# Kernel optimization log

Hardware: AMD Instinct MI355X
Metric: run time of the kernel (lower is better)

Reference implementation:

```python
import jax, jax.numpy as jnp
import numpy as np

N_NODES = 50000
N_EDGES = 400000
IN_DIM, HID, OUT_DIM = 24, 256, 12


def _sage_conv(x, src, dst, w_l, b_l, w_r, num_nodes):
    # PyG SAGEConv (aggr='mean', root_weight=True):
    #   out = lin_l(mean_{j in N(i)} x_j) + lin_r(x_i)
    msg = x[src]                                             # [E, H] gather
    s = jax.ops.segment_sum(msg, dst, num_segments=num_nodes)  # [N, H]
    cnt = jax.ops.segment_sum(jnp.ones((src.shape[0],), x.dtype), dst,
                              num_segments=num_nodes)          # [N]
    mean = s / jnp.maximum(cnt, 1.0)[:, None]
    return mean @ w_l + b_l + x @ w_r


def setup_inputs() -> dict:
    key = jax.random.key(0)
    ks = jax.random.split(key, 16)
    sc = 0.05
    inp = {
        "x": jax.random.normal(ks[0], (N_NODES, IN_DIM), jnp.float32),
        "edge_index": jax.random.randint(ks[1], (2, N_EDGES), 0, N_NODES, jnp.int64),
        # encoder: Linear(24,128) ReLU Linear(128,256) ReLU
        "enc_w1": sc * jax.random.normal(ks[2], (IN_DIM, HID // 2), jnp.float32),
        "enc_b1": jnp.zeros((HID // 2,), jnp.float32),
        "enc_w2": sc * jax.random.normal(ks[3], (HID // 2, HID), jnp.float32),
        "enc_b2": jnp.zeros((HID,), jnp.float32),
        # SAGEConv 1 / 2: lin_l (with bias) on aggregated, lin_r (no bias) on root
        "s1_wl": sc * jax.random.normal(ks[4], (HID, HID), jnp.float32),
        "s1_bl": jnp.zeros((HID,), jnp.float32),
        "s1_wr": sc * jax.random.normal(ks[5], (HID, HID), jnp.float32),
        "s2_wl": sc * jax.random.normal(ks[6], (HID, HID), jnp.float32),
        "s2_bl": jnp.zeros((HID,), jnp.float32),
        "s2_wr": sc * jax.random.normal(ks[7], (HID, HID), jnp.float32),
        # readout: Linear(256,128) ReLU Linear(128,12)
        "ro_w1": sc * jax.random.normal(ks[8], (HID, HID // 2), jnp.float32),
        "ro_b1": jnp.zeros((HID // 2,), jnp.float32),
        "ro_w2": sc * jax.random.normal(ks[9], (HID // 2, OUT_DIM), jnp.float32),
        "ro_b2": jnp.zeros((OUT_DIM,), jnp.float32),
    }
    return inp


def reference(x, edge_index, enc_w1, enc_b1, enc_w2, enc_b2,
              s1_wl, s1_bl, s1_wr, s2_wl, s2_bl, s2_wr,
              ro_w1, ro_b1, ro_w2, ro_b2):
    n = x.shape[0]
    src, dst = edge_index[0], edge_index[1]
    # encoder MLP
    h = jax.nn.relu(x @ enc_w1 + enc_b1)
    h = jax.nn.relu(h @ enc_w2 + enc_b2)
    # two SAGE layers with ReLU
    h = jax.nn.relu(_sage_conv(h, src, dst, s1_wl, s1_bl, s1_wr, n))
    h = jax.nn.relu(_sage_conv(h, src, dst, s2_wl, s2_bl, s2_wr, n))
    # readout MLP
    h = jax.nn.relu(h @ ro_w1 + ro_b1)
    return h @ ro_w2 + ro_b2
```

## Files before the change

kernel.cpp:

```cpp
#include <hip/hip_runtime.h>
#include <hip/hip_bf16.h>

#define N_NODES 50000
#define N_EDGES 400000
#define IN_DIM 24
#define HID 256
#define OUT_DIM 12

typedef _Float16 fp16_t;
typedef __attribute__((ext_vector_type(8))) _Float16 half8;
typedef __attribute__((ext_vector_type(4))) float f32x4;

__device__ __forceinline__ void gload_lds16(const void* g, void* l) {
    typedef __attribute__((address_space(3))) unsigned int u32_lds;
    typedef const __attribute__((address_space(1))) unsigned int u32_glb;
    __builtin_amdgcn_global_load_lds((u32_glb*)(unsigned long long)g,
                                     (u32_lds*)(unsigned int)(unsigned long long)l,
                                     16, 0, 0);
}

template<int K, int M, int ROWS>
__global__ __launch_bounds__(M) void lin_enc1(const float* __restrict__ X,
                                              const float* __restrict__ W,
                                              const float* __restrict__ b,
                                              fp16_t* __restrict__ Y, int N) {
    __shared__ float xs[ROWS][K];
    const int row0 = blockIdx.x * ROWS;
    const int tid = threadIdx.x;
    for (int i = tid; i < ROWS * K; i += M) {
        int r = i / K, k = i - r * K;
        int gr = row0 + r;
        xs[r][k] = (gr < N) ? X[(long long)gr * K + k] : 0.f;
    }
    __syncthreads();
    const int j = tid;
    float acc[ROWS];
    float bj = b[j];
#pragma unroll
    for (int r = 0; r < ROWS; ++r) acc[r] = bj;
    for (int k = 0; k < K; ++k) {
        float w = W[k * M + j];
#pragma unroll
        for (int r = 0; r < ROWS; ++r) acc[r] = fmaf(xs[r][k], w, acc[r]);
    }
#pragma unroll
    for (int r = 0; r < ROWS; ++r) {
        int gr = row0 + r;
        if (gr < N) {
            float v = fmaxf(acc[r], 0.f);
            Y[(size_t)gr * M + j] = (fp16_t)v;
        }
    }
}

__global__ __launch_bounds__(256) void wtrans_all(
    const float* __restrict__ enc_w2,
    const float* __restrict__ s1_wl, const float* __restrict__ s1_wr,
    const float* __restrict__ s2_wl, const float* __restrict__ s2_wr,
    const float* __restrict__ ro_w1,
    fp16_t* __restrict__ wtE,
    fp16_t* __restrict__ wtS1,
    fp16_t* __restrict__ wtS2,
    fp16_t* __restrict__ wtR) {
    const int sE = 256 * 128, sS = 256 * 512, sR = 128 * 256;
    int idx = blockIdx.x * blockDim.x + threadIdx.x;
    float v; fp16_t* p; int o;
    if (idx < sE) {
        int j = idx / 128, k = idx - j * 128;
        v = enc_w2[(size_t)k * 256 + j]; p = wtE; o = idx;
    } else if (idx < sE + sS) {
        int t = idx - sE; int j = t / 512, k = t - j * 512;
        v = (k < 256) ? s1_wl[(size_t)k * 256 + j] : s1_wr[(size_t)(k - 256) * 256 + j];
        p = wtS1; o = t;
    } else if (idx < sE + 2 * sS) {
        int t = idx - sE - sS; int j = t / 512, k = t - j * 512;
        v = (k < 256) ? s2_wl[(size_t)k * 256 + j] : s2_wr[(size_t)(k - 256) * 256 + j];
        p = wtS2; o = t;
    } else if (idx < sE + 2 * sS + sR) {
        int t = idx - sE - 2 * sS; int j = t / 256, k = t - j * 256;
        v = ro_w1[(size_t)k * 128 + j]; p = wtR; o = t;
    } else return;
    p[o] = (fp16_t)v;
}

template<int K, int MODE, int BM, int BN, bool WF32, bool WH16, bool RELU>
__global__ __launch_bounds__((BM / 64) * (BN / 64) * 64, 4) void gemm_mfma(
    const fp16_t* __restrict__ A, const fp16_t* __restrict__ A2,
    const fp16_t* __restrict__ W,
    const float* __restrict__ bias,
    float* __restrict__ Yf, fp16_t* __restrict__ Yh,
    int N, int M) {
    constexpr int NWR = BM / 64;
    constexpr int NWC = BN / 64;
    constexpr int NT = NWR * NWC * 64;
    __shared__ __align__(16) fp16_t ldsA[BM * 32];
    __shared__ __align__(16) fp16_t ldsB[BN * 32];
    const int tid = threadIdx.x;
    const int r0 = blockIdx.x * BM;
    const int j0 = blockIdx.y * BN;
    const int w = tid >> 6, lane = tid & 63;
    const int wr = w / NWC, wc = w % NWC;
    const int lrow = lane & 15, lg = lane >> 4;

    f32x4 acc[4][4] = {};

    for (int kc = 0; kc < K; kc += 32) {
        __syncthreads();
        const fp16_t* pa;
        int ka, KA;
        if (MODE == 1) {
            KA = HID;
            if (kc >= HID) { pa = A2; ka = kc - HID; }
            else           { pa = A;  ka = kc; }
        } else {
            KA = K; pa = A; ka = kc;
        }
#pragma unroll
        for (int c = tid; c < BM * 4; c += NT) {
            int row = c >> 2, p = c & 3;
            int g = (p - (row >> 1)) & 3;
            int gr = r0 + row; if (gr > N - 1) gr = N - 1;
            gload_lds16(pa + (size_t)gr * KA + ka + g * 8,
                        (char*)ldsA + (size_t)c * 16);
        }
#pragma unroll
        for (int c = tid; c < BN * 4; c += NT) {
            int row = c >> 2, p = c & 3;
            int g = (p - (row >> 1)) & 3;
            gload_lds16(W + (size_t)(j0 + row) * K + kc + g * 8,
                        (char*)ldsB + (size_t)c * 16);
        }
        __syncthreads();

        half8 a[4], b[4];
#pragma unroll
        for (int f = 0; f < 4; ++f) {
            int ar = wr * 64 + f * 16 + lrow;
            int sa = (lg + (ar >> 1)) & 3;
            a[f] = *(const half8*)&ldsA[ar * 32 + sa * 8];
            int br = wc * 64 + f * 16 + lrow;
            int sb = (lg + (br >> 1)) & 3;
            b[f] = *(const half8*)&ldsB[br * 32 + sb * 8];
        }
#pragma unroll
        for (int fi = 0; fi < 4; ++fi)
#pragma unroll
            for (int fj = 0; fj < 4; ++fj)
                acc[fi][fj] = __builtin_amdgcn_mfma_f32_16x16x32_f16(a[fi], b[fj], acc[fi][fj], 0, 0, 0);
    }

#pragma unroll
    for (int fj = 0; fj < 4; ++fj) {
        int ocol = j0 + wc * 64 + fj * 16 + lrow;
        float bv = bias[ocol];
#pragma unroll
        for (int fi = 0; fi < 4; ++fi) {
#pragma unroll
            for (int r = 0; r < 4; ++r) {
                int orow = r0 + wr * 64 + fi * 16 + lg * 4 + r;
                if (orow < N) {
                    float v = acc[fi][fj][r] + bv;
                    if (RELU) v = fmaxf(v, 0.f);
                    size_t o = (size_t)orow * M + ocol;
                    if (WF32) Yf[o] = v;
                    if (WH16) Yh[o] = (fp16_t)v;
                }
            }
        }
    }
}

__global__ __launch_bounds__(1024) void zero_kernel(int* __restrict__ p, int n) {
    int i = blockIdx.x * blockDim.x + threadIdx.x;
    if (i < n) p[i] = 0;
}

__global__ void deg_kernel(const int* __restrict__ dst, int* __restrict__ deg, int E) {
    int e = blockIdx.x * blockDim.x + threadIdx.x;
    if (e < E) atomicAdd(&deg[dst[e]], 1);
}

__global__ __launch_bounds__(256) void scan_local(const int* __restrict__ deg,
                                                  int* __restrict__ locincl,
                                                  int* __restrict__ bsum, int N) {
    const int t = threadIdx.x;
    const int i = blockIdx.x * 256 + t;
    int v = (i < N) ? deg[i] : 0;
    const int lane = t & 63;
    int x = v;
#pragma unroll
    for (int off = 1; off < 64; off <<= 1) {
        int y = __shfl_up(x, off, 64);
        if (lane >= off) x += y;
    }
    __shared__ int wsum[4];
    if (lane == 63) wsum[t >> 6] = x;
    __syncthreads();
    const int wid = t >> 6;
    int add = 0;
    for (int wI = 0; wI < wid; ++wI) add += wsum[wI];
    x += add;
    if (i < N) locincl[i] = x;
    if (t == 255) bsum[blockIdx.x] = x;
}

__global__ __launch_bounds__(256) void scan_bsum(int* __restrict__ bsum, int B) {
    const int t = threadIdx.x;
    int v = (t < B) ? bsum[t] : 0;
    const int lane = t & 63;
    int x = v;
#pragma unroll
    for (int off = 1; off < 64; off <<= 1) {
        int y = __shfl_up(x, off, 64);
        if (lane >= off) x += y;
    }
    __shared__ int wsum[4];
    if (lane == 63) wsum[t >> 6] = x;
    __syncthreads();
    const int wid = t >> 6;
    int add = 0;
    for (int wI = 0; wI < wid; ++wI) add += wsum[wI];
    x += add;
    if (t < B) bsum[t] = x - v;
}

__global__ __launch_bounds__(256) void scan_final(const int* __restrict__ deg,
                                                  const int* __restrict__ locincl,
                                                  const int* __restrict__ bsum,
                                                  int* __restrict__ rowptr,
                                                  int* __restrict__ cursor, int N, int E) {
    const int i = blockIdx.x * 256 + threadIdx.x;
    if (i < N) {
        int excl = bsum[blockIdx.x] + locincl[i] - deg[i];
        rowptr[i] = excl;
        cursor[i] = excl;
    }
    if (i == 0) rowptr[N] = E;
}

__global__ void scatter_kernel(const int* __restrict__ src, const int* __restrict__ dst,
                               int* __restrict__ cursor, int* __restrict__ esrc, int E) {
    int e = blockIdx.x * blockDim.x + threadIdx.x;
    if (e < E) {
        int pos = atomicAdd(&cursor[dst[e]], 1);
        esrc[pos] = src[e];
    }
}

__global__ __launch_bounds__(256) void agg_csr(const fp16_t* __restrict__ h,
                                               const int* __restrict__ rowptr,
                                               const int* __restrict__ esrc,
                                               fp16_t* __restrict__ mean, int N) {
    const int n = blockIdx.x * 4 + (threadIdx.x >> 6);
    if (n >= N) return;
    const int lane = threadIdx.x & 63;
    const int half = lane >> 5;
    const int l32 = lane & 31;
    const int r0 = rowptr[n];
    const int r1 = rowptr[n + 1];
    const int deg = r1 - r0;

    float acc[8];
#pragma unroll
    for (int j = 0; j < 8; ++j) acc[j] = 0.f;

    for (int e = r0 + half; e < r1; e += 2) {
        int s = esrc[e];
        half8 v = *(const half8*)&h[(size_t)s * HID + l32 * 8];
#pragma unroll
        for (int j = 0; j < 8; ++j) acc[j] += (float)v[j];
    }
#pragma unroll
    for (int j = 0; j < 8; ++j) acc[j] += __shfl(acc[j], lane ^ 32, 64);

    if (half == 0) {
        float inv = 1.0f / fmaxf((float)deg, 1.0f);
        half8 o;
#pragma unroll
        for (int j = 0; j < 8; ++j) o[j] = (fp16_t)(acc[j] * inv);
        *(half8*)&mean[(size_t)n * HID + l32 * 8] = o;
    }
}

__global__ void lin_final(const float* __restrict__ X, const float* __restrict__ W,
                          const float* __restrict__ b, float* __restrict__ Y, int N) {
    int idx = blockIdx.x * blockDim.x + threadIdx.x;
    if (idx >= N * OUT_DIM) return;
    int row = idx / OUT_DIM;
    int j = idx - row * OUT_DIM;
    float acc = b[j];
#pragma unroll 8
    for (int k = 0; k < 128; ++k)
        acc = fmaf(X[row * 128 + k], W[k * OUT_DIM + j], acc);
    Y[idx] = acc;
}

extern "C" void kernel_launch(void* const* d_in, const int* in_sizes, int n_in,
                              void* d_out, int out_size, void* d_ws, size_t ws_size,
                              hipStream_t stream) {
    const float* x      = (const float*)d_in[0];
    const int*   eidx   = (const int*)d_in[1];
    const float* enc_w1 = (const float*)d_in[2];
    const float* enc_b1 = (const float*)d_in[3];
    const float* enc_w2 = (const float*)d_in[4];
    const float* enc_b2 = (const float*)d_in[5];
    const float* s1_wl  = (const float*)d_in[6];
    const float* s1_bl  = (const float*)d_in[7];
    const float* s1_wr  = (const float*)d_in[8];
    const float* s2_wl  = (const float*)d_in[9];
    const float* s2_bl  = (const float*)d_in[10];
    const float* s2_wr  = (const float*)d_in[11];
    const float* ro_w1  = (const float*)d_in[12];
    const float* ro_b1  = (const float*)d_in[13];
    const float* ro_w2  = (const float*)d_in[14];
    const float* ro_b2  = (const float*)d_in[15];
    float* out = (float*)d_out;

    const int N = N_NODES;
    const int E = N_EDGES;
    const int* src = eidx;
    const int* dst = eidx + E;

    char* ws = (char*)d_ws;
    size_t off = 0;
    auto alloc = [&](size_t bytes) { void* p = ws + off; off += (bytes + 255) & ~255ULL; return p; };
    int* deg     = (int*)alloc((size_t)N * 4);
    int* rowptr  = (int*)alloc((size_t)(N + 1) * 4);
    int* cursor  = (int*)alloc((size_t)N * 4);
    int* esrc    = (int*)alloc((size_t)E * 4);
    int* locincl = (int*)alloc((size_t)N * 4);
    int* bsum    = (int*)alloc((size_t)256 * 4);
    fp16_t* wtE  = (fp16_t*)alloc((size_t)256 * 128 * 2);
    fp16_t* wtS1 = (fp16_t*)alloc((size_t)256 * 512 * 2);
    fp16_t* wtS2 = (fp16_t*)alloc((size_t)256 * 512 * 2);
    fp16_t* wtR  = (fp16_t*)alloc((size_t)128 * 256 * 2);
    fp16_t* h0   = (fp16_t*)alloc((size_t)N * 128 * 2);
    float* f32buf = (float*)alloc((size_t)N * 128 * 4);
    fp16_t* hA   = (fp16_t*)alloc((size_t)N * HID * 2);
    fp16_t* hB   = (fp16_t*)alloc((size_t)N * HID * 2);
    fp16_t* mbuf = (fp16_t*)alloc((size_t)N * HID * 2);

    const int nb8 = (N + 7) / 8;
    const int gx128 = (N + 127) / 128;
    const int nbScan = (N + 255) / 256;
    const int nbAgg = (N + 3) / 4;
    const int wtTot = 256 * 128 + 2 * 256 * 512 + 128 * 256;

    zero_kernel<<<(N + 1023) / 1024, 1024, 0, stream>>>(deg, N);
    deg_kernel<<<(E + 255) / 256, 256, 0, stream>>>(dst, deg, E);
    scan_local<<<nbScan, 256, 0, stream>>>(deg, locincl, bsum, N);
    scan_bsum<<<1, 256, 0, stream>>>(bsum, nbScan);
    scan_final<<<nbScan, 256, 0, stream>>>(deg, locincl, bsum, rowptr, cursor, N, E);
    scatter_kernel<<<(E + 255) / 256, 256, 0, stream>>>(src, dst, cursor, esrc, E);

    wtrans_all<<<(wtTot + 255) / 256, 256, 0, stream>>>(
        enc_w2, s1_wl, s1_wr, s2_wl, s2_wr, ro_w1, wtE, wtS1, wtS2, wtR);

    lin_enc1<IN_DIM, 128, 8><<<nb8, 128, 0, stream>>>(x, enc_w1, enc_b1, h0, N);
    gemm_mfma<128, 0, 128, 256, false, true, true><<<dim3(gx128, 1), 512, 0, stream>>>(
        h0, nullptr, wtE, enc_b2, nullptr, hA, N, 256);

    agg_csr<<<nbAgg, 256, 0, stream>>>(hA, rowptr, esrc, mbuf, N);
    gemm_mfma<512, 1, 128, 256, false, true, true><<<dim3(gx128, 1), 512, 0, stream>>>(
        mbuf, hA, wtS1, s1_bl, nullptr, hB, N, 256);

    agg_csr<<<nbAgg, 256, 0, stream>>>(hB, rowptr, esrc, mbuf, N);
    gemm_mfma<512, 1, 128, 256, false, true, true><<<dim3(gx128, 1), 512, 0, stream>>>(
        mbuf, hB, wtS2, s2_bl, nullptr, hA, N, 256);

    gemm_mfma<256, 0, 128, 128, true, false, true><<<dim3(gx128, 1), 256, 0, stream>>>(
        hA, nullptr, wtR, ro_b1, f32buf, nullptr, N, 128);
    lin_final<<<(N * OUT_DIM + 255) / 256, 256, 0, stream>>>(f32buf, ro_w2, ro_b2, out, N);
}
```

Measured before the change: 259.5 us.

## Fuse readout MLP into one MFMA kernel and fold deg zeroing into weight transpose

Replaces the readout GEMM (which wrote a 50000x128 fp32 intermediate) and the scalar lin_final kernel with one kernel. It keeps the ReLU hidden tile in swizzled LDS as fp16 and runs the 128->12 projection with MFMA against a padded transposed W2. It also removes the separate zero kernel by clearing deg inside wtrans_all, which now launches first. This removes an intermediate round trip to global memory and two launches, but adds LDS pressure (about 48KB per block) and rounds the second-layer inputs and weights to fp16.

```diff
diff --git a/kernel.cpp b/kernel.cpp
--- a/kernel.cpp
+++ b/kernel.cpp
@@ -61,9 +61,11 @@
     fp16_t* __restrict__ wtE,
     fp16_t* __restrict__ wtS1,
     fp16_t* __restrict__ wtS2,
-    fp16_t* __restrict__ wtR) {
+    fp16_t* __restrict__ wtR,
+    int* __restrict__ deg, int N) {
     const int sE = 256 * 128, sS = 256 * 512, sR = 128 * 256;
     int idx = blockIdx.x * blockDim.x + threadIdx.x;
+    if (idx < N) deg[idx] = 0;
     float v; fp16_t* p; int o;
     if (idx < sE) {
         int j = idx / 128, k = idx - j * 128;
@@ -83,12 +85,12 @@
     p[o] = (fp16_t)v;
 }
 
-template<int K, int MODE, int BM, int BN, bool WF32, bool WH16, bool RELU>
+template<int K, int MODE, int BM, int BN, bool WH16, bool RELU>
 __global__ __launch_bounds__((BM / 64) * (BN / 64) * 64, 4) void gemm_mfma(
     const fp16_t* __restrict__ A, const fp16_t* __restrict__ A2,
     const fp16_t* __restrict__ W,
     const float* __restrict__ bias,
-    float* __restrict__ Yf, fp16_t* __restrict__ Yh,
+    fp16_t* __restrict__ Yh,
     int N, int M) {
     constexpr int NWR = BM / 64;
     constexpr int NWC = BN / 64;
@@ -161,18 +163,118 @@
                 if (orow < N) {
                     float v = acc[fi][fj][r] + bv;
                     if (RELU) v = fmaxf(v, 0.f);
-                    size_t o = (size_t)orow * M + ocol;
-                    if (WF32) Yf[o] = v;
-                    if (WH16) Yh[o] = (fp16_t)v;
+                    if (WH16) Yh[(size_t)orow * M + ocol] = (fp16_t)v;
                 }
             }
         }
     }
 }
 
-__global__ __launch_bounds__(1024) void zero_kernel(int* __restrict__ p, int n) {
-    int i = blockIdx.x * blockDim.x + threadIdx.x;
-    if (i < n) p[i] = 0;
+__global__ __launch_bounds__(256, 3) void gemm_ro(
+    const fp16_t* __restrict__ A,
+    const fp16_t* __restrict__ W,
+    const float* __restrict__ b1,
+    const float* __restrict__ W2,
+    const float* __restrict__ b2,
+    float* __restrict__ out, int N) {
+    constexpr int K = 256;
+    __shared__ __align__(16) fp16_t ldsA[128 * 32];
+    __shared__ __align__(16) fp16_t ldsB[128 * 32];
+    __shared__ __align__(16) fp16_t htile[128 * 128];
+    __shared__ __align__(16) fp16_t w2t[16 * 128];
+    const int tid = threadIdx.x;
+    const int r0 = blockIdx.x * 128;
+    const int w = tid >> 6, lane = tid & 63;
+    const int wr = w >> 1, wc = w & 1;
+    const int lrow = lane & 15, lg = lane >> 4;
+
+    for (int i = tid; i < 16 * 128; i += 256) {
+        int c = i >> 7, k = i & 127;
+        w2t[i] = (c < 12) ? (fp16_t)W2[k * 12 + c] : (fp16_t)0.f;
+    }
+
+    f32x4 acc[4][4] = {};
+    for (int kc = 0; kc < K; kc += 32) {
+        __syncthreads();
+#pragma unroll
+        for (int c = tid; c < 128 * 4; c += 256) {
+            int row = c >> 2, p = c & 3;
+            int g = (p - (row >> 1)) & 3;
+            int gr = r0 + row; if (gr > N - 1) gr = N - 1;
+            gload_lds16(A + (size_t)gr * K + kc + g * 8, (char*)ldsA + (size_t)c * 16);
+        }
+#pragma unroll
+        for (int c = tid; c < 128 * 4; c += 256) {
+            int row = c >> 2, p = c & 3;
+            int g = (p - (row >> 1)) & 3;
+            gload_lds16(W + (size_t)row * K + kc + g * 8, (char*)ldsB + (size_t)c * 16);
+        }
+        __syncthreads();
+
+        half8 a[4], b[4];
+#pragma unroll
+        for (int f = 0; f < 4; ++f) {
+            int ar = wr * 64 + f * 16 + lrow;
+            int sa = (lg + (ar >> 1)) & 3;
+            a[f] = *(const half8*)&ldsA[ar * 32 + sa * 8];
+            int br = wc * 64 + f * 16 + lrow;
+            int sb = (lg + (br >> 1)) & 3;
+            b[f] = *(const half8*)&ldsB[br * 32 + sb * 8];
+        }
+#pragma unroll
+        for (int fi = 0; fi < 4; ++fi)
+#pragma unroll
+            for (int fj = 0; fj < 4; ++fj)
+                acc[fi][fj] = __builtin_amdgcn_mfma_f32_16x16x32_f16(a[fi], b[fj], acc[fi][fj], 0, 0, 0);
+    }
+
+#pragma unroll
+    for (int fj = 0; fj < 4; ++fj) {
+        int ocol = wc * 64 + fj * 16 + lrow;
+        float bv = b1[ocol];
+        int q = ocol >> 3;
+#pragma unroll
+        for (int fi = 0; fi < 4; ++fi) {
+#pragma unroll
+            for (int r = 0; r < 4; ++r) {
+                int orow = wr * 64 + fi * 16 + lg * 4 + r;
+                float v = fmaxf(acc[fi][fj][r] + bv, 0.f);
+                int phys = (q + (orow >> 1)) & 15;
+                htile[orow * 128 + phys * 8 + (ocol & 7)] = (fp16_t)v;
+            }
+        }
+    }
+    __syncthreads();
+
+    if (w < 2) {
+        f32x4 accF[4] = {};
+#pragma unroll
+        for (int kt = 0; kt < 4; ++kt) {
+            half8 bb = *(const half8*)&w2t[lrow * 128 + kt * 32 + lg * 8];
+            half8 a[4];
+#pragma unroll
+            for (int f = 0; f < 4; ++f) {
+                int ar = w * 64 + f * 16 + lrow;
+                int q = kt * 4 + lg;
+                int phys = (q + (ar >> 1)) & 15;
+                a[f] = *(const half8*)&htile[ar * 128 + phys * 8];
+            }
+#pragma unroll
+            for (int f = 0; f < 4; ++f)
+                accF[f] = __builtin_amdgcn_mfma_f32_16x16x32_f16(a[f], bb, accF[f], 0, 0, 0);
+        }
+        if (lrow < OUT_DIM) {
+            float bv = b2[lrow];
+#pragma unroll
+            for (int f = 0; f < 4; ++f) {
+#pragma unroll
+                for (int r = 0; r < 4; ++r) {
+                    int orow = r0 + w * 64 + f * 16 + lg * 4 + r;
+                    if (orow < N) out[(size_t)orow * OUT_DIM + lrow] = accF[f][r] + bv;
+                }
+            }
+        }
+    }
 }
 
 __global__ void deg_kernel(const int* __restrict__ dst, int* __restrict__ deg, int E) {
@@ -280,19 +382,6 @@
         for (int j = 0; j < 8; ++j) o[j] = (fp16_t)(acc[j] * inv);
         *(half8*)&mean[(size_t)n * HID + l32 * 8] = o;
     }
-}
-
-__global__ void lin_final(const float* __restrict__ X, const float* __restrict__ W,
-                          const float* __restrict__ b, float* __restrict__ Y, int N) {
-    int idx = blockIdx.x * blockDim.x + threadIdx.x;
-    if (idx >= N * OUT_DIM) return;
-    int row = idx / OUT_DIM;
-    int j = idx - row * OUT_DIM;
-    float acc = b[j];
-#pragma unroll 8
-    for (int k = 0; k < 128; ++k)
-        acc = fmaf(X[row * 128 + k], W[k * OUT_DIM + j], acc);
-    Y[idx] = acc;
 }
 
 extern "C" void kernel_launch(void* const* d_in, const int* in_sizes, int n_in,
@@ -335,7 +424,6 @@
     fp16_t* wtS2 = (fp16_t*)alloc((size_t)256 * 512 * 2);
     fp16_t* wtR  = (fp16_t*)alloc((size_t)128 * 256 * 2);
     fp16_t* h0   = (fp16_t*)alloc((size_t)N * 128 * 2);
-    float* f32buf = (float*)alloc((size_t)N * 128 * 4);
     fp16_t* hA   = (fp16_t*)alloc((size_t)N * HID * 2);
     fp16_t* hB   = (fp16_t*)alloc((size_t)N * HID * 2);
     fp16_t* mbuf = (fp16_t*)alloc((size_t)N * HID * 2);
@@ -346,29 +434,26 @@
     const int nbAgg = (N + 3) / 4;
     const int wtTot = 256 * 128 + 2 * 256 * 512 + 128 * 256;
 
-    zero_kernel<<<(N + 1023) / 1024, 1024, 0, stream>>>(deg, N);
+    wtrans_all<<<(wtTot + 255) / 256, 256, 0, stream>>>(
+        enc_w2, s1_wl, s1_wr, s2_wl, s2_wr, ro_w1, wtE, wtS1, wtS2, wtR, deg, N);
+
     deg_kernel<<<(E + 255) / 256, 256, 0, stream>>>(dst, deg, E);
     scan_local<<<nbScan, 256, 0, stream>>>(deg, locincl, bsum, N);
     scan_bsum<<<1, 256, 0, stream>>>(bsum, nbScan);
     scan_final<<<nbScan, 256, 0, stream>>>(deg, locincl, bsum, rowptr, cursor, N, E);
     scatter_kernel<<<(E + 255) / 256, 256, 0, stream>>>(src, dst, cursor, esrc, E);
 
-    wtrans_all<<<(wtTot + 255) / 256, 256, 0, stream>>>(
-        enc_w2, s1_wl, s1_wr, s2_wl, s2_wr, ro_w1, wtE, wtS1, wtS2, wtR);
-
     lin_enc1<IN_DIM, 128, 8><<<nb8, 128, 0, stream>>>(x, enc_w1, enc_b1, h0, N);
-    gemm_mfma<128, 0, 128, 256, false, true, true><<<dim3(gx128, 1), 512, 0, stream>>>(
-        h0, nullptr, wtE, enc_b2, nullptr, hA, N, 256);
+    gemm_mfma<128, 0, 128, 256, true, true><<<dim3(gx128, 1), 512, 0, stream>>>(
+        h0, nullptr, wtE, enc_b2, hA, N, 256);
 
     agg_csr<<<nbAgg, 256, 0, stream>>>(hA, rowptr, esrc, mbuf, N);
-    gemm_mfma<512, 1, 128, 256, false, true, true><<<dim3(gx128, 1), 512, 0, stream>>>(
-        mbuf, hA, wtS1, s1_bl, nullptr, hB, N, 256);
+    gemm_mfma<512, 1, 128, 256, true, true><<<dim3(gx128, 1), 512, 0, stream>>>(
+        mbuf, hA, wtS1, s1_bl, hB, N, 256);
 
     agg_csr<<<nbAgg, 256, 0, stream>>>(hB, rowptr, esrc, mbuf, N);
-    gemm_mfma<512, 1, 128, 256, false, true, true><<<dim3(gx128, 1), 512, 0, stream>>>(
-        mbuf, hB, wtS2, s2_bl, nullptr, hA, N, 256);
-
-    gemm_mfma<256, 0, 128, 128, true, false, true><<<dim3(gx128, 1), 256, 0, stream>>>(
-        hA, nullptr, wtR, ro_b1, f32buf, nullptr, N, 128);
-    lin_final<<<(N * OUT_DIM + 255) / 256, 256, 0, stream>>>(f32buf, ro_w2, ro_b2, out, N);
-}
+    gemm_mfma<512, 1, 128, 256, true, true><<<dim3(gx128, 1), 512, 0, stream>>>(
+        mbuf, hB, wtS2, s2_bl, hA, N, 256);
+
+    gemm_ro<<<gx128, 256, 0, stream>>>(hA, wtR, ro_b1, ro_w2, ro_b2, out, N);
+}
```

Result: faster. 229.9 us (-11.4%).
